# Optimization experiments

Measured on AMD Instinct MI355X. Metric: run time of the kernel, lower is better.

## Reference

```python
import jax, jax.numpy as jnp
import numpy as np

B, C_IMG, H, W = 64, 256, 64, 64
HID, T = 512, 128
M, A = 128, 128  # multifeat_size, attfeat_size


def setup_inputs() -> dict:
    key = jax.random.key(0)
    ks = jax.random.split(key, 9)
    s = 0.02
    return {
        "img_feat": jax.random.normal(ks[0], (B, C_IMG, H, W), jnp.float32),
        "text_feat": jax.random.normal(ks[1], (B, HID, T), jnp.float32),
        "W_img": jax.random.normal(ks[2], (M, C_IMG), jnp.float32) * s,   # in_img_conv 1x1
        "W_txt": jax.random.normal(ks[3], (M, HID), jnp.float32) * s,     # in_text_conv 1d k=1
        "W_qfc": jax.random.normal(ks[4], (A, M), jnp.float32) * s,       # multi_qfc
        "W_ifc": jax.random.normal(ks[5], (A, M), jnp.float32) * s,       # multi_ifc
        "W_ipc": jax.random.normal(ks[6], (A, M), jnp.float32) * s,       # ifeat_proj_conv 1x1
        "W_qpc": jax.random.normal(ks[7], (A, M), jnp.float32) * s,       # qfeat_proj_conv 1x1
        "W_att": jax.random.normal(ks[8], (1, A), jnp.float32) * s,       # att_conv 1x1
    }


def reference(img_feat, text_feat, W_img, W_txt, W_qfc, W_ifc, W_ipc, W_qpc, W_att):
    b, c, h, w = img_feat.shape
    n = h * w  # conv_feat_num
    x = img_feat.reshape(b, c, n)
    # in_img_conv: dropout(id) -> 1x1 conv -> tanh ; in_text_conv analogous
    in_ifeat = jnp.tanh(jnp.einsum("mc,bcn->bmn", W_img, x))        # [B,M,HW]
    in_qfeat = jnp.tanh(jnp.einsum("mh,bht->bmt", W_txt, text_feat))  # [B,M,T]

    # text-guided image attention branch
    qfeatatt = jnp.mean(in_qfeat, axis=2) @ W_qfc.T                  # [B,A]
    ifeatproj = jnp.einsum("am,bmn->ban", W_ipc, in_ifeat)           # [B,A,HW]
    addfeat_i = jnp.tanh(qfeatatt[:, :, None] + ifeatproj)

    # image-guided text attention branch
    ifeatatt = jnp.mean(in_ifeat, axis=2) @ W_ifc.T                  # [B,A]
    qfeatproj = jnp.einsum("am,bmt->bat", W_qpc, in_qfeat)           # [B,A,T]
    addfeat_q = jnp.tanh(ifeatatt[:, :, None] + qfeatproj)

    attfeat_join = jnp.concatenate([addfeat_i, addfeat_q], axis=2)   # [B,A,HW+T]
    att_logits = jnp.einsum("a,ban->bn", W_att[0], attfeat_join)     # [B,HW+T]
    att = jax.nn.softmax(att_logits, axis=1)

    joint_feat = jnp.concatenate([in_ifeat, in_qfeat], axis=2)       # [B,M,HW+T]
    att_feat = jnp.einsum("bmn,bn->bm", joint_feat, att)             # [B,M]
    return att_feat, att
```

## Files before the change

kernel.cpp:

```cpp
#include <hip/hip_runtime.h>
#include <hip/hip_bf16.h>

#define DI static __device__ __forceinline__

typedef unsigned short u16;
typedef unsigned int   u32;
typedef __bf16 bf16_t;
typedef __bf16 bf16x8 __attribute__((ext_vector_type(8)));
typedef float  f32x4  __attribute__((ext_vector_type(4)));

union BF8 { ushort4 u4[2]; bf16x8 v; };

DI u16 f2bf(float f) { union { bf16_t b; u16 u; } c; c.b = (bf16_t)f; return c.u; }
DI float bf2f(u32 lo) { union { u32 u; float f; } c; c.u = lo << 16; return c.f; }
DI float fast_tanh(float x) { float e = __expf(2.0f * x); return 1.0f - 2.0f / (e + 1.0f); }

constexpr int NB   = 64;
constexpr int CIMG = 256;
constexpr int HID  = 512;
constexpr int HW   = 4096;
constexpr int TT   = 128;
constexpr int NTOT = HW + TT;

constexpr size_t WS_WIMG  = 0;
constexpr size_t WS_WTXT  = WS_WIMG  + 128ull*256*2;
constexpr size_t WS_WIPC  = WS_WTXT  + 128ull*512*2;
constexpr size_t WS_WQPC  = WS_WIPC  + 128ull*128*2;
constexpr size_t WS_IFEAT = WS_WQPC  + 128ull*128*2;
constexpr size_t WS_QFEAT = WS_IFEAT + (size_t)NB*128*HW*2;
constexpr size_t WS_QFP   = WS_QFEAT + (size_t)NB*128*TT*2;
constexpr size_t WS_LOGIT = WS_QFP   + (size_t)NB*128*TT*4;
constexpr size_t WS_ISUM  = WS_LOGIT + (size_t)NB*NTOT*4;
constexpr size_t WS_QSUM  = WS_ISUM  + (size_t)NB*128*4;
constexpr size_t WS_QATT  = WS_QSUM  + (size_t)NB*128*4;

__global__ void k_zero(float* __restrict__ p, int n) {
    int i = blockIdx.x * 256 + threadIdx.x;
    if (i < n) p[i] = 0.0f;
}

__global__ void k_convert(const float* __restrict__ s, bf16_t* __restrict__ d, int n) {
    int i = blockIdx.x * 256 + threadIdx.x;
    if (i < n) d[i] = (bf16_t)s[i];
}

__global__ void k_qatt(const float* __restrict__ qsum, const float* __restrict__ Wqfc,
                       float* __restrict__ qatt) {
    int b = blockIdx.x, a = threadIdx.x;
    const float* qs = qsum + b * 128;
    const float* wr = Wqfc + a * 128;
    float s = 0.f;
    for (int m = 0; m < 128; ++m) s += qs[m] * wr[m];
    qatt[b * 128 + a] = s * (1.0f / 128.0f);
}

__global__ void k_textlogits(const float* __restrict__ isum, const float* __restrict__ Wifc,
                             const float* __restrict__ Watt, const float* __restrict__ qfp,
                             float* __restrict__ logits) {
    int b = blockIdx.x, tid = threadIdx.x;
    __shared__ float ia[128];
    __shared__ float wat[128];
    __shared__ float part[2][128];
    if (tid < 128) {
        float s = 0.f;
        const float* is = isum + b * 128;
        const float* wr = Wifc + tid * 128;
        for (int m = 0; m < 128; ++m) s += is[m] * wr[m];
        ia[tid]  = s * (1.0f / 4096.0f);
        wat[tid] = Watt[tid];
    }
    __syncthreads();
    int t = tid & 127, h = tid >> 7;
    const float* qp = qfp + ((size_t)b * 128 + h * 64) * 128 + t;
    float s = 0.f;
    for (int a0 = 0; a0 < 64; ++a0) {
        int a = h * 64 + a0;
        s += wat[a] * fast_tanh(ia[a] + qp[(size_t)a0 * 128]);
    }
    part[h][t] = s;
    __syncthreads();
    if (tid < 128) logits[b * NTOT + 4096 + tid] = part[0][tid] + part[1][tid];
}

__global__ void k_softmax(const float* __restrict__ logits, float* __restrict__ att) {
    int b = blockIdx.x, tid = threadIdx.x;
    const float* L = logits + (size_t)b * NTOT;
    float* O = att + (size_t)b * NTOT;
    __shared__ float red[4];
    __shared__ float red2[4];
    float mx = -3.0e38f;
    for (int i = tid; i < NTOT; i += 256) mx = fmaxf(mx, L[i]);
    for (int off = 1; off < 64; off <<= 1) mx = fmaxf(mx, __shfl_xor(mx, off, 64));
    if ((tid & 63) == 0) red[tid >> 6] = mx;
    __syncthreads();
    mx = fmaxf(fmaxf(red[0], red[1]), fmaxf(red[2], red[3]));
    float s = 0.f;
    for (int i = tid; i < NTOT; i += 256) {
        float e = __expf(L[i] - mx);
        O[i] = e;
        s += e;
    }
    for (int off = 1; off < 64; off <<= 1) s += __shfl_xor(s, off, 64);
    if ((tid & 63) == 0) red2[tid >> 6] = s;
    __syncthreads();
    float inv = 1.0f / (red2[0] + red2[1] + red2[2] + red2[3]);
    for (int i = tid; i < NTOT; i += 256) O[i] *= inv;
}

__global__ void k_attfeat(const bf16_t* __restrict__ ifeat, const bf16_t* __restrict__ qfeat,
                          const float* __restrict__ att, float* __restrict__ out) {
    int mg = blockIdx.x;
    int b  = blockIdx.y;
    int tid = threadIdx.x;
    const u16* F = (const u16*)ifeat + ((size_t)b * 128 + mg * 8) * HW;
    const u16* Q = (const u16*)qfeat + ((size_t)b * 128 + mg * 8) * TT;
    const float* A_ = att + (size_t)b * NTOT;
    float acc[8] = {0, 0, 0, 0, 0, 0, 0, 0};
    for (int i = tid; i < HW / 2; i += 256) {
        float2 a2 = *(const float2*)&A_[2 * i];
#pragma unroll
        for (int r = 0; r < 8; ++r) {
            u32 pk = *(const u32*)&F[(size_t)r * HW + 2 * i];
            acc[r] += bf2f(pk & 0xffffu) * a2.x + bf2f(pk >> 16) * a2.y;
        }
    }
    for (int i = tid; i < TT / 2; i += 256) {
        float2 a2 = *(const float2*)&A_[HW + 2 * i];
#pragma unroll
        for (int r = 0; r < 8; ++r) {
            u32 pk = *(const u32*)&Q[(size_t)r * TT + 2 * i];
            acc[r] += bf2f(pk & 0xffffu) * a2.x + bf2f(pk >> 16) * a2.y;
        }
    }
    __shared__ float red[4][8];
    int lane = tid & 63, wv = tid >> 6;
#pragma unroll
    for (int r = 0; r < 8; ++r) {
        float s = acc[r];
        s += __shfl_xor(s, 1, 64);
        s += __shfl_xor(s, 2, 64);
        s += __shfl_xor(s, 4, 64);
        s += __shfl_xor(s, 8, 64);
        s += __shfl_xor(s, 16, 64);
        s += __shfl_xor(s, 32, 64);
        if (lane == 0) red[wv][r] = s;
    }
    __syncthreads();
    if (tid < 8)
        out[(size_t)b * 128 + mg * 8 + tid] = red[0][tid] + red[1][tid] + red[2][tid] + red[3][tid];
}

template <int C, bool IMG>
__global__ __launch_bounds__(256) void k_chain(
    const float* __restrict__ xin, const bf16_t* __restrict__ Wa, const bf16_t* __restrict__ Wp,
    const float* __restrict__ qatt, const float* __restrict__ Watt, bf16_t* __restrict__ feat_out,
    float* __restrict__ sums, float* __restrict__ proj_out, int S) {
    constexpr int LDX = C + 4;
    __shared__ u16 Xl[64 * LDX];
    __shared__ u16 Y1[64 * 132];
    __shared__ u16 Y1N[128 * 68];
    __shared__ float lred[4][64];
    __shared__ float qf_l[128];
    __shared__ float wa_l[128];

    const int tid = threadIdx.x;
    const int b  = blockIdx.y;
    const int n0 = blockIdx.x * 64;
    const int l  = tid & 63, w = tid >> 6;
    const int lr = l & 15, g = l >> 4;

    if constexpr (IMG) {
        if (tid < 128) {
            qf_l[tid] = qatt[b * 128 + tid];
            wa_l[tid] = Watt[tid];
        }
    }

    {
        const int col = tid & 63, cg = tid >> 6;
        constexpr int CQ = C / 4;
        const float* xb = xin + (size_t)b * C * S + n0 + col;
#pragma unroll 4
        for (int i = 0; i < CQ; i += 4) {
            int c = cg * CQ + i;
            float f0 = xb[(size_t)(c + 0) * S];
            float f1 = xb[(size_t)(c + 1) * S];
            float f2 = xb[(size_t)(c + 2) * S];
            float f3 = xb[(size_t)(c + 3) * S];
            ushort4 p4;
            p4.x = f2bf(f0); p4.y = f2bf(f1); p4.z = f2bf(f2); p4.w = f2bf(f3);
            *(ushort4*)&Xl[col * LDX + c] = p4;
        }
    }
    __syncthreads();

    f32x4 acc1[2][4];
#pragma unroll
    for (int rt = 0; rt < 2; ++rt)
#pragma unroll
        for (int ct = 0; ct < 4; ++ct)
#pragma unroll
            for (int r = 0; r < 4; ++r) acc1[rt][ct][r] = 0.f;

    const bf16_t* wa0 = Wa + (size_t)(w * 32 + lr) * C + g * 8;
#pragma unroll
    for (int ks = 0; ks < C / 32; ++ks) {
        bf16x8 af0 = *(const bf16x8*)(wa0 + ks * 32);
        bf16x8 af1 = *(const bf16x8*)(wa0 + (size_t)16 * C + ks * 32);
#pragma unroll
        for (int ct = 0; ct < 4; ++ct) {
            BF8 bu;
            const u16* p = &Xl[(ct * 16 + lr) * LDX + ks * 32 + g * 8];
            bu.u4[0] = *(const ushort4*)p;
            bu.u4[1] = *(const ushort4*)(p + 4);
            acc1[0][ct] = __builtin_amdgcn_mfma_f32_16x16x32_bf16(af0, bu.v, acc1[0][ct], 0, 0, 0);
            acc1[1][ct] = __builtin_amdgcn_mfma_f32_16x16x32_bf16(af1, bu.v, acc1[1][ct], 0, 0, 0);
        }
    }

    float y[2][4][4];
#pragma unroll
    for (int rt = 0; rt < 2; ++rt)
#pragma unroll
        for (int ct = 0; ct < 4; ++ct)
#pragma unroll
            for (int r = 0; r < 4; ++r) y[rt][ct][r] = fast_tanh(acc1[rt][ct][r]);

#pragma unroll
    for (int rt = 0; rt < 2; ++rt)
#pragma unroll
        for (int r = 0; r < 4; ++r) {
            float s = y[rt][0][r] + y[rt][1][r] + y[rt][2][r] + y[rt][3][r];
            s += __shfl_xor(s, 1, 64);
            s += __shfl_xor(s, 2, 64);
            s += __shfl_xor(s, 4, 64);
            s += __shfl_xor(s, 8, 64);
            if (lr == 0) atomicAdd(&sums[b * 128 + w * 32 + rt * 16 + g * 4 + r], s);
        }

#pragma unroll
    for (int rt = 0; rt < 2; ++rt)
#pragma unroll
        for (int ct = 0; ct < 4; ++ct) {
            int m0 = w * 32 + rt * 16 + g * 4;
            int c2 = ct * 16 + lr;
#pragma unroll
            for (int r = 0; r < 4; r += 2) {
                u32 pk = (u32)f2bf(y[rt][ct][r]) | ((u32)f2bf(y[rt][ct][r + 1]) << 16);
                *(u32*)&Y1[c2 * 132 + m0 + r] = pk;
            }
#pragma unroll
            for (int r = 0; r < 4; ++r) Y1N[(m0 + r) * 68 + c2] = f2bf(y[rt][ct][r]);
        }
    __syncthreads();

    f32x4 acc2[2][4];
#pragma unroll
    for (int rt = 0; rt < 2; ++rt)
#pragma unroll
        for (int ct = 0; ct < 4; ++ct)
#pragma unroll
            for (int r = 0; r < 4; ++r) acc2[rt][ct][r] = 0.f;

    const bf16_t* wp0 = Wp + (size_t)(w * 32 + lr) * 128 + g * 8;
#pragma unroll
    for (int ks = 0; ks < 4; ++ks) {
        bf16x8 af0 = *(const bf16x8*)(wp0 + ks * 32);
        bf16x8 af1 = *(const bf16x8*)(wp0 + 16 * 128 + ks * 32);
#pragma unroll
        for (int ct = 0; ct < 4; ++ct) {
            BF8 bu;
            const u16* p = &Y1[(ct * 16 + lr) * 132 + ks * 32 + g * 8];
            bu.u4[0] = *(const ushort4*)p;
            bu.u4[1] = *(const ushort4*)(p + 4);
            acc2[0][ct] = __builtin_amdgcn_mfma_f32_16x16x32_bf16(af0, bu.v, acc2[0][ct], 0, 0, 0);
            acc2[1][ct] = __builtin_amdgcn_mfma_f32_16x16x32_bf16(af1, bu.v, acc2[1][ct], 0, 0, 0);
        }
    }

    {
        u16* fb = (u16*)feat_out + (size_t)b * 128 * S + n0;
#pragma unroll
        for (int it = 0; it < 8; ++it) {
            int m = w * 32 + it * 4 + g;
            int nc = lr * 4;
            ushort4 v = *(const ushort4*)&Y1N[m * 68 + nc];
            *(ushort4*)(fb + (size_t)m * S + nc) = v;
        }
    }

    if constexpr (IMG) {
        float ps[4] = {0, 0, 0, 0};
#pragma unroll
        for (int rt = 0; rt < 2; ++rt)
#pragma unroll
            for (int r = 0; r < 4; ++r) {
                int a = w * 32 + rt * 16 + g * 4 + r;
                float qa = qf_l[a], wv = wa_l[a];
#pragma unroll
                for (int ct = 0; ct < 4; ++ct) ps[ct] += wv * fast_tanh(qa + acc2[rt][ct][r]);
            }
#pragma unroll
        for (int ct = 0; ct < 4; ++ct) {
            ps[ct] += __shfl_xor(ps[ct], 16, 64);
            ps[ct] += __shfl_xor(ps[ct], 32, 64);
        }
        if (g == 0) {
#pragma unroll
            for (int ct = 0; ct < 4; ++ct) lred[w][ct * 16 + lr] = ps[ct];
        }
        __syncthreads();
        if (tid < 64)
            proj_out[(size_t)b * NTOT + n0 + tid] =
                lred[0][tid] + lred[1][tid] + lred[2][tid] + lred[3][tid];
    } else {
#pragma unroll
        for (int rt = 0; rt < 2; ++rt)
#pragma unroll
            for (int ct = 0; ct < 4; ++ct) {
                int a = w * 32 + rt * 16 + g * 4;
                int t = n0 + ct * 16 + lr;
#pragma unroll
                for (int r = 0; r < 4; ++r)
                    proj_out[((size_t)b * 128 + a + r) * 128 + t] = acc2[rt][ct][r];
            }
    }
}

extern "C" void kernel_launch(void* const* d_in, const int* in_sizes, int n_in, void* d_out,
                              int out_size, void* d_ws, size_t ws_size, hipStream_t stream) {
    (void)in_sizes; (void)n_in; (void)out_size; (void)ws_size;
    const float* img  = (const float*)d_in[0];
    const float* txt  = (const float*)d_in[1];
    const float* Wimg = (const float*)d_in[2];
    const float* Wtxt = (const float*)d_in[3];
    const float* Wqfc = (const float*)d_in[4];
    const float* Wifc = (const float*)d_in[5];
    const float* Wipc = (const float*)d_in[6];
    const float* Wqpc = (const float*)d_in[7];
    const float* Watt = (const float*)d_in[8];

    char* ws = (char*)d_ws;
    bf16_t* wimg_b  = (bf16_t*)(ws + WS_WIMG);
    bf16_t* wtxt_b  = (bf16_t*)(ws + WS_WTXT);
    bf16_t* wipc_b  = (bf16_t*)(ws + WS_WIPC);
    bf16_t* wqpc_b  = (bf16_t*)(ws + WS_WQPC);
    bf16_t* ifeat_b = (bf16_t*)(ws + WS_IFEAT);
    bf16_t* qfeat_b = (bf16_t*)(ws + WS_QFEAT);
    float*  qfp     = (float*)(ws + WS_QFP);
    float*  logits  = (float*)(ws + WS_LOGIT);
    float*  isum    = (float*)(ws + WS_ISUM);
    float*  qsum    = (float*)(ws + WS_QSUM);
    float*  qatt    = (float*)(ws + WS_QATT);

    float* out_feat = (float*)d_out;
    float* out_att  = (float*)d_out + 64 * 128;

    k_zero<<<(2 * 64 * 128 + 255) / 256, 256, 0, stream>>>(isum, 2 * 64 * 128);

    int n1 = 128 * 256, n2 = 128 * 512, n3 = 128 * 128;
    k_convert<<<(n1 + 255) / 256, 256, 0, stream>>>(Wimg, wimg_b, n1);
    k_convert<<<(n2 + 255) / 256, 256, 0, stream>>>(Wtxt, wtxt_b, n2);
    k_convert<<<(n3 + 255) / 256, 256, 0, stream>>>(Wipc, wipc_b, n3);
    k_convert<<<(n3 + 255) / 256, 256, 0, stream>>>(Wqpc, wqpc_b, n3);

    k_chain<512, false><<<dim3(2, 64), 256, 0, stream>>>(txt, wtxt_b, wqpc_b, nullptr, nullptr,
                                                         qfeat_b, qsum, qfp, TT);
    k_qatt<<<64, 128, 0, stream>>>(qsum, Wqfc, qatt);
    k_chain<256, true><<<dim3(64, 64), 256, 0, stream>>>(img, wimg_b, wipc_b, qatt, Watt,
                                                         ifeat_b, isum, logits, HW);
    k_textlogits<<<64, 256, 0, stream>>>(isum, Wifc, Watt, qfp, logits);
    k_softmax<<<64, 256, 0, stream>>>(logits, out_att);
    k_attfeat<<<dim3(16, 64), 256, 0, stream>>>(ifeat_b, qfeat_b, out_att, out_feat);
}
```

Baseline: 503.3 us.

## Chunk chain input staging, share LDS buffer, split attfeat, fuse weight converts

```diff
diff --git a/kernel.cpp b/kernel.cpp
--- a/kernel.cpp
+++ b/kernel.cpp
@@ -16,8 +16,6 @@
 DI float fast_tanh(float x) { float e = __expf(2.0f * x); return 1.0f - 2.0f / (e + 1.0f); }
 
 constexpr int NB   = 64;
-constexpr int CIMG = 256;
-constexpr int HID  = 512;
 constexpr int HW   = 4096;
 constexpr int TT   = 128;
 constexpr int NTOT = HW + TT;
@@ -39,9 +37,18 @@
     if (i < n) p[i] = 0.0f;
 }
 
-__global__ void k_convert(const float* __restrict__ s, bf16_t* __restrict__ d, int n) {
+__global__ void k_convert4(const float* __restrict__ s0, const float* __restrict__ s1,
+                           const float* __restrict__ s2, const float* __restrict__ s3,
+                           bf16_t* __restrict__ d0, bf16_t* __restrict__ d1,
+                           bf16_t* __restrict__ d2, bf16_t* __restrict__ d3) {
     int i = blockIdx.x * 256 + threadIdx.x;
-    if (i < n) d[i] = (bf16_t)s[i];
+    if (i < 32768) { d0[i] = (bf16_t)s0[i]; return; }
+    i -= 32768;
+    if (i < 65536) { d1[i] = (bf16_t)s1[i]; return; }
+    i -= 65536;
+    if (i < 16384) { d2[i] = (bf16_t)s2[i]; return; }
+    i -= 16384;
+    d3[i] = (bf16_t)s3[i];
 }
 
 __global__ void k_qatt(const float* __restrict__ qsum, const float* __restrict__ Wqfc,
@@ -110,13 +117,17 @@
 __global__ void k_attfeat(const bf16_t* __restrict__ ifeat, const bf16_t* __restrict__ qfeat,
                           const float* __restrict__ att, float* __restrict__ out) {
     int mg = blockIdx.x;
-    int b  = blockIdx.y;
+    int ns = blockIdx.y;
+    int b  = blockIdx.z;
     int tid = threadIdx.x;
     const u16* F = (const u16*)ifeat + ((size_t)b * 128 + mg * 8) * HW;
     const u16* Q = (const u16*)qfeat + ((size_t)b * 128 + mg * 8) * TT;
     const float* A_ = att + (size_t)b * NTOT;
     float acc[8] = {0, 0, 0, 0, 0, 0, 0, 0};
-    for (int i = tid; i < HW / 2; i += 256) {
+    int i0 = ns * 512;
+#pragma unroll
+    for (int it = 0; it < 2; ++it) {
+        int i = i0 + it * 256 + tid;
         float2 a2 = *(const float2*)&A_[2 * i];
 #pragma unroll
         for (int r = 0; r < 8; ++r) {
@@ -124,11 +135,11 @@
             acc[r] += bf2f(pk & 0xffffu) * a2.x + bf2f(pk >> 16) * a2.y;
         }
     }
-    for (int i = tid; i < TT / 2; i += 256) {
-        float2 a2 = *(const float2*)&A_[HW + 2 * i];
+    if (ns == 0 && tid < TT / 2) {
+        float2 a2 = *(const float2*)&A_[HW + 2 * tid];
 #pragma unroll
         for (int r = 0; r < 8; ++r) {
-            u32 pk = *(const u32*)&Q[(size_t)r * TT + 2 * i];
+            u32 pk = *(const u32*)&Q[(size_t)r * TT + 2 * tid];
             acc[r] += bf2f(pk & 0xffffu) * a2.x + bf2f(pk >> 16) * a2.y;
         }
     }
@@ -147,18 +158,18 @@
     }
     __syncthreads();
     if (tid < 8)
-        out[(size_t)b * 128 + mg * 8 + tid] = red[0][tid] + red[1][tid] + red[2][tid] + red[3][tid];
+        atomicAdd(&out[(size_t)b * 128 + mg * 8 + tid],
+                  red[0][tid] + red[1][tid] + red[2][tid] + red[3][tid]);
 }
 
 template <int C, bool IMG>
-__global__ __launch_bounds__(256) void k_chain(
+__global__ __launch_bounds__(256, 4) void k_chain(
     const float* __restrict__ xin, const bf16_t* __restrict__ Wa, const bf16_t* __restrict__ Wp,
     const float* __restrict__ qatt, const float* __restrict__ Watt, bf16_t* __restrict__ feat_out,
     float* __restrict__ sums, float* __restrict__ proj_out, int S) {
-    constexpr int LDX = C + 4;
-    __shared__ u16 Xl[64 * LDX];
+    constexpr int NCH = C / 128;
+    __shared__ u16 XY[128 * 68];
     __shared__ u16 Y1[64 * 132];
-    __shared__ u16 Y1N[128 * 68];
     __shared__ float lred[4][64];
     __shared__ float qf_l[128];
     __shared__ float wa_l[128];
@@ -176,24 +187,6 @@
         }
     }
 
-    {
-        const int col = tid & 63, cg = tid >> 6;
-        constexpr int CQ = C / 4;
-        const float* xb = xin + (size_t)b * C * S + n0 + col;
-#pragma unroll 4
-        for (int i = 0; i < CQ; i += 4) {
-            int c = cg * CQ + i;
-            float f0 = xb[(size_t)(c + 0) * S];
-            float f1 = xb[(size_t)(c + 1) * S];
-            float f2 = xb[(size_t)(c + 2) * S];
-            float f3 = xb[(size_t)(c + 3) * S];
-            ushort4 p4;
-            p4.x = f2bf(f0); p4.y = f2bf(f1); p4.z = f2bf(f2); p4.w = f2bf(f3);
-            *(ushort4*)&Xl[col * LDX + c] = p4;
-        }
-    }
-    __syncthreads();
-
     f32x4 acc1[2][4];
 #pragma unroll
     for (int rt = 0; rt < 2; ++rt)
@@ -203,19 +196,42 @@
             for (int r = 0; r < 4; ++r) acc1[rt][ct][r] = 0.f;
 
     const bf16_t* wa0 = Wa + (size_t)(w * 32 + lr) * C + g * 8;
-#pragma unroll
-    for (int ks = 0; ks < C / 32; ++ks) {
-        bf16x8 af0 = *(const bf16x8*)(wa0 + ks * 32);
-        bf16x8 af1 = *(const bf16x8*)(wa0 + (size_t)16 * C + ks * 32);
-#pragma unroll
-        for (int ct = 0; ct < 4; ++ct) {
-            BF8 bu;
-            const u16* p = &Xl[(ct * 16 + lr) * LDX + ks * 32 + g * 8];
-            bu.u4[0] = *(const ushort4*)p;
-            bu.u4[1] = *(const ushort4*)(p + 4);
-            acc1[0][ct] = __builtin_amdgcn_mfma_f32_16x16x32_bf16(af0, bu.v, acc1[0][ct], 0, 0, 0);
-            acc1[1][ct] = __builtin_amdgcn_mfma_f32_16x16x32_bf16(af1, bu.v, acc1[1][ct], 0, 0, 0);
-        }
+    const int colb = (tid & 15) * 4;
+    const int r0   = tid >> 4;
+
+    for (int h = 0; h < NCH; ++h) {
+        {
+            const float* xb = xin + (size_t)b * C * S + (size_t)h * 128 * S + n0 + colb;
+#pragma unroll
+            for (int p = 0; p < 8; ++p) {
+                int c2 = p * 16 + r0;
+                float4 f = *(const float4*)(xb + (size_t)c2 * S);
+                u16 v[4] = {f2bf(f.x), f2bf(f.y), f2bf(f.z), f2bf(f.w)};
+                int rot = c2 & 3;
+#pragma unroll
+                for (int s = 0; s < 4; ++s) {
+                    int jj = (s + rot) & 3;
+                    XY[(colb + jj) * 132 + c2] = v[jj];
+                }
+            }
+        }
+        __syncthreads();
+#pragma unroll
+        for (int ks2 = 0; ks2 < 4; ++ks2) {
+            int ks = h * 4 + ks2;
+            bf16x8 af0 = *(const bf16x8*)(wa0 + ks * 32);
+            bf16x8 af1 = *(const bf16x8*)(wa0 + (size_t)16 * C + ks * 32);
+#pragma unroll
+            for (int ct = 0; ct < 4; ++ct) {
+                BF8 bu;
+                const u16* p = &XY[(ct * 16 + lr) * 132 + ks2 * 32 + g * 8];
+                bu.u4[0] = *(const ushort4*)p;
+                bu.u4[1] = *(const ushort4*)(p + 4);
+                acc1[0][ct] = __builtin_amdgcn_mfma_f32_16x16x32_bf16(af0, bu.v, acc1[0][ct], 0, 0, 0);
+                acc1[1][ct] = __builtin_amdgcn_mfma_f32_16x16x32_bf16(af1, bu.v, acc1[1][ct], 0, 0, 0);
+            }
+        }
+        __syncthreads();
     }
 
     float y[2][4][4];
@@ -250,7 +266,7 @@
                 *(u32*)&Y1[c2 * 132 + m0 + r] = pk;
             }
 #pragma unroll
-            for (int r = 0; r < 4; ++r) Y1N[(m0 + r) * 68 + c2] = f2bf(y[rt][ct][r]);
+            for (int r = 0; r < 4; ++r) XY[(m0 + r) * 68 + c2] = f2bf(y[rt][ct][r]);
         }
     __syncthreads();
 
@@ -284,7 +300,7 @@
         for (int it = 0; it < 8; ++it) {
             int m = w * 32 + it * 4 + g;
             int nc = lr * 4;
-            ushort4 v = *(const ushort4*)&Y1N[m * 68 + nc];
+            ushort4 v = *(const ushort4*)&XY[m * 68 + nc];
             *(ushort4*)(fb + (size_t)m * S + nc) = v;
         }
     }
@@ -357,12 +373,10 @@
     float* out_att  = (float*)d_out + 64 * 128;
 
     k_zero<<<(2 * 64 * 128 + 255) / 256, 256, 0, stream>>>(isum, 2 * 64 * 128);
-
-    int n1 = 128 * 256, n2 = 128 * 512, n3 = 128 * 128;
-    k_convert<<<(n1 + 255) / 256, 256, 0, stream>>>(Wimg, wimg_b, n1);
-    k_convert<<<(n2 + 255) / 256, 256, 0, stream>>>(Wtxt, wtxt_b, n2);
-    k_convert<<<(n3 + 255) / 256, 256, 0, stream>>>(Wipc, wipc_b, n3);
-    k_convert<<<(n3 + 255) / 256, 256, 0, stream>>>(Wqpc, wqpc_b, n3);
+    k_zero<<<(64 * 128 + 255) / 256, 256, 0, stream>>>(out_feat, 64 * 128);
+
+    k_convert4<<<131072 / 256, 256, 0, stream>>>(Wimg, Wtxt, Wipc, Wqpc,
+                                                 wimg_b, wtxt_b, wipc_b, wqpc_b);
 
     k_chain<512, false><<<dim3(2, 64), 256, 0, stream>>>(txt, wtxt_b, wqpc_b, nullptr, nullptr,
                                                          qfeat_b, qsum, qfp, TT);
@@ -371,5 +385,5 @@
                                                          ifeat_b, isum, logits, HW);
     k_textlogits<<<64, 256, 0, stream>>>(isum, Wifc, Watt, qfp, logits);
     k_softmax<<<64, 256, 0, stream>>>(logits, out_att);
-    k_attfeat<<<dim3(16, 64), 256, 0, stream>>>(ifeat_b, qfeat_b, out_att, out_feat);
-}
+    k_attfeat<<<dim3(16, 4, 64), 256, 0, stream>>>(ifeat_b, qfeat_b, out_att, out_feat);
+}
```

Measured after the change: 491.8 us. 2.3% less time.
